# Kernel optimization log

Hardware: AMD Instinct MI355X
Metric: run time of the kernel (lower is better)

## Reference

```python
import jax, jax.numpy as jnp
import numpy as np

B, N = 4, 20                        # batch, qubits
L = int(np.ceil(np.log2(N)))        # 5 layers, one 4x4 generator each


def setup_inputs():
    key = jax.random.key(0)
    k1, k2, k3, k4 = jax.random.split(key, 4)
    psi_re = jax.random.normal(k1, (B, 2 ** N), dtype=jnp.float32)
    psi_im = jax.random.normal(k2, (B, 2 ** N), dtype=jnp.float32)
    nrm = jnp.sqrt(jnp.sum(psi_re ** 2 + psi_im ** 2, axis=1, keepdims=True))
    psi_re, psi_im = psi_re / nrm, psi_im / nrm   # normalized quantum state
    H_re = jax.random.normal(k3, (L, 4, 4), dtype=jnp.float32)
    H_im = jax.random.normal(k4, (L, 4, 4), dtype=jnp.float32)
    return {"psi_re": psi_re, "psi_im": psi_im, "H_re": H_re, "H_im": H_im}


def _make_unitary(A):
    # torch.matrix_exp(A - A^H): expm of an anti-Hermitian generator via eigh
    G = A - A.conj().T
    w, V = jnp.linalg.eigh(-1j * G)            # G = i * Hermitian
    return (V * jnp.exp(1j * w)) @ V.conj().T  # expm(G), unitary


def _apply_gate(T, U4, axes):
    # contract 4x4 gate (reshaped [2,2,2,2]) onto two qubit axes of tensor T
    T = jnp.tensordot(U4, T, axes=((2, 3), axes))
    return jnp.moveaxis(T, (0, 1), axes)


def _gate_pairs(nq):
    pairs = [(2 * i, 2 * i + 1) for i in range(nq // 2)]
    if nq > 2:
        pairs += [(2 * i + 1, (2 * i + 2) % nq) for i in range(nq // 2)]
    return pairs


def _forward(psi_re, psi_im, H_re, H_im):
    psi = (psi_re + 1j * psi_im).astype(jnp.complex64).reshape((B,) + (2,) * N)
    H = (H_re + 1j * H_im).astype(jnp.complex64)
    state, is_dm, nq = psi, False, N
    for layer in range(L):
        U = _make_unitary(H[layer]).reshape(2, 2, 2, 2)
        Uc = U.conj()
        # _2local_conv: brick pattern of the same 2-qubit gate
        for (a, b) in _gate_pairs(nq):
            state = _apply_gate(state, U, (1 + a, 1 + b))
            if is_dm:  # density matrix: also apply U* on bra axes
                state = _apply_gate(state, Uc, (1 + nq + a, 1 + nq + b))
        # _2local_pool: measuring qubits 0..nq//2-1 with index shifting removes
        # the even-indexed qubits -> partial trace over them
        if nq >= 2:
            traced = [2 * i for i in range(nq // 2)]
            kept = [q for q in range(nq) if q not in traced]
            t, k = len(traced), len(kept)
            if is_dm:
                perm = (0,) + tuple(1 + q for q in kept) + tuple(1 + q for q in traced) \
                     + tuple(1 + nq + q for q in kept) + tuple(1 + nq + q for q in traced)
                r = jnp.transpose(state, perm).reshape(B, 2 ** k, 2 ** t, 2 ** k, 2 ** t)
                state = jnp.einsum('bitjt->bij', r).reshape((B,) + (2,) * k + (2,) * k)
            else:
                perm = (0,) + tuple(1 + q for q in traced) + tuple(1 + q for q in kept)
                p = jnp.transpose(state, perm).reshape(B, 2 ** t, 2 ** k)
                state = jnp.einsum('bti,btj->bij', p, p.conj()).reshape((B,) + (2,) * k + (2,) * k)
                is_dm = True
            nq = k
    # final state.measure(0): reduced 1-qubit density matrix, take P(outcome 0)
    r = state.reshape(B, 2, 2 ** (nq - 1), 2, 2 ** (nq - 1))
    rho0 = jnp.einsum('birjr->bij', r)
    return rho0[:, 0, 0].real


def reference(psi_re, psi_im, H_re, H_im):
    return _forward(psi_re, psi_im, H_re, H_im)
```

## Files before the change

### kernel.cpp

```cpp
#include <hip/hip_runtime.h>
#include <math.h>


__device__ __forceinline__ float2 cmul(float2 a, float2 b) {
  return make_float2(a.x * b.x - a.y * b.y, a.x * b.y + a.y * b.x);
}
__device__ __forceinline__ float2 cmadd(float2 acc, float2 a, float2 b) {
  acc.x = fmaf(a.x, b.x, fmaf(-a.y, b.y, acc.x));
  acc.y = fmaf(a.x, b.y, fmaf(a.y, b.x, acc.y));
  return acc;
}
__device__ __forceinline__ float2 cmaddc(float2 acc, float2 a, float2 b) {
  acc.x = fmaf(a.x, b.x, fmaf(a.y, b.y, acc.x));
  acc.y = fmaf(a.y, b.x, fmaf(-a.x, b.y, acc.y));
  return acc;
}
__device__ __forceinline__ int pad(int e) { return e + (e >> 4); }

__device__ __forceinline__ unsigned spread(unsigned v) {
  v = (v | (v << 8)) & 0x00FF00FFu;
  v = (v | (v << 4)) & 0x0F0F0F0Fu;
  v = (v | (v << 2)) & 0x33333333u;
  v = (v | (v << 1)) & 0x55555555u;
  return v;
}
__device__ __forceinline__ unsigned spread2(unsigned v) { return spread(spread(v)); }
__device__ __forceinline__ int ins(int x, int p) {
  return ((x >> p) << (p + 1)) | (x & ((1 << p) - 1));
}

__device__ __forceinline__ void gate4(float2& v0, float2& v1, float2& v2, float2& v3,
                                      const float2 (&U)[16]) {
  float2 n0 = cmul(U[0], v0);  n0 = cmadd(n0, U[1], v1);  n0 = cmadd(n0, U[2], v2);  n0 = cmadd(n0, U[3], v3);
  float2 n1 = cmul(U[4], v0);  n1 = cmadd(n1, U[5], v1);  n1 = cmadd(n1, U[6], v2);  n1 = cmadd(n1, U[7], v3);
  float2 n2 = cmul(U[8], v0);  n2 = cmadd(n2, U[9], v1);  n2 = cmadd(n2, U[10], v2); n2 = cmadd(n2, U[11], v3);
  float2 n3 = cmul(U[12], v0); n3 = cmadd(n3, U[13], v1); n3 = cmadd(n3, U[14], v2); n3 = cmadd(n3, U[15], v3);
  v0 = n0; v1 = n1; v2 = n2; v3 = n3;
}

__device__ __forceinline__ void gate16(float2 (&v)[16], const float2 (&U)[16]) {
#pragma unroll
  for (int g = 0; g < 4; g++)
    gate4(v[g * 4 + 0], v[g * 4 + 1], v[g * 4 + 2], v[g * 4 + 3], U);
#pragma unroll
  for (int lo = 0; lo < 4; lo++)
    gate4(v[lo], v[lo + 4], v[lo + 8], v[lo + 12], U);
}

__device__ __forceinline__ void apply_gate_tile13(float2* t, const float2 (&U)[16],
                                                  int pa, int pb, int tid) {
  int p0 = pa < pb ? pa : pb;
  int p1 = pa < pb ? pb : pa;
  int m0 = (1 << p0) - 1, m1 = (1 << p1) - 1;
  int ia = 1 << pa, ib = 1 << pb;
#pragma unroll
  for (int g = tid; g < 2048; g += 256) {
    int idx = ((g & ~m0) << 1) | (g & m0);
    idx = ((idx & ~m1) << 1) | (idx & m1);
    int e0 = pad(idx), e1 = pad(idx | ib), e2 = pad(idx | ia), e3 = pad(idx | ia | ib);
    float2 v0 = t[e0], v1 = t[e1], v2 = t[e2], v3 = t[e3];
    gate4(v0, v1, v2, v3, U);
    t[e0] = v0; t[e1] = v1; t[e2] = v2; t[e3] = v3;
  }
}

__device__ __forceinline__ void phase4_l0(float2* t, const float2 (&U)[16],
                                          int p0, int p1, int p2, int p3, int tid) {
  int o0 = 1 << p0, o1 = 1 << p1, o2 = 1 << p2, o3 = 1 << p3;
#pragma unroll
  for (int it = 0; it < 2; it++) {
    int h = tid + it * 256;
    int idx = ins(ins(ins(ins(h, p0), p1), p2), p3);
    float2 v[16];
#pragma unroll
    for (int j = 0; j < 16; j++) {
      int off = ((j & 1) ? o0 : 0) + ((j & 2) ? o1 : 0) + ((j & 4) ? o2 : 0) + ((j & 8) ? o3 : 0);
      v[j] = t[pad(idx + off)];
    }
    gate16(v, U);
#pragma unroll
    for (int j = 0; j < 16; j++) {
      int off = ((j & 1) ? o0 : 0) + ((j & 2) ? o1 : 0) + ((j & 4) ? o2 : 0) + ((j & 8) ? o3 : 0);
      t[pad(idx + off)] = v[j];
    }
  }
}

__device__ __forceinline__ void phase4_pool(float2* w, const float2 (&U)[16],
                                            int a_lo, int a_hi, int c_lo, int c_hi,
                                            int o0, int o1, int o2, int o3, int tid) {
#pragma unroll
  for (int it = 0; it < 2; it++) {
    int h = tid + it * 256;
    int uu = h & 7, ss = (h >> 3) & 7, t_lo = h >> 6;
    int u = ins(ins(uu, a_lo), a_hi);
    int s = ins(ins(ss, c_lo), c_hi);
    int base = t_lo * 1056 + s * 33 + u;
    float2 v[16];
#pragma unroll
    for (int j = 0; j < 16; j++) {
      int off = ((j & 1) ? o0 : 0) + ((j & 2) ? o1 : 0) + ((j & 4) ? o2 : 0) + ((j & 8) ? o3 : 0);
      v[j] = w[base + off];
    }
    gate16(v, U);
#pragma unroll
    for (int j = 0; j < 16; j++) {
      int off = ((j & 1) ? o0 : 0) + ((j & 2) ? o1 : 0) + ((j & 4) ? o2 : 0) + ((j & 8) ? o3 : 0);
      w[base + off] = v[j];
    }
  }
}

__device__ __forceinline__ void gate_su(float2* w, const float2 (&U)[16],
                                        int a, int c, int offa, int offb, int tid) {
#pragma unroll
  for (int g = tid; g < 2048; g += 256) {
    int uu = g & 15, ss = (g >> 4) & 15, t_lo = g >> 8;
    int u = ins(uu, a), s = ins(ss, c);
    int base = t_lo * 1056 + s * 33 + u;
    float2 v0 = w[base], v1 = w[base + offb], v2 = w[base + offa], v3 = w[base + offa + offb];
    gate4(v0, v1, v2, v3, U);
    w[base] = v0; w[base + offb] = v1; w[base + offa] = v2; w[base + offa + offb] = v3;
  }
}

__global__ __launch_bounds__(320) void expm_kernel(const float* __restrict__ Hre,
                                                   const float* __restrict__ Him,
                                                   float2* __restrict__ Uout) {
  int wave = threadIdx.x >> 6;
  int lane = threadIdx.x & 63;
  if (wave >= 5 || lane >= 16) return;
  int l = wave;
  int r = lane >> 2, c = lane & 3;
  double tr = (double)Hre[l * 16 + r * 4 + c] - (double)Hre[l * 16 + c * 4 + r];
  double ti = (double)Him[l * 16 + r * 4 + c] + (double)Him[l * 16 + c * 4 + r];
  double a = sqrt(tr * tr + ti * ti);
  a += __shfl_xor(a, 1, 64);
  a += __shfl_xor(a, 2, 64);
  double nrm = fmax(a, __shfl_xor(a, 4, 64));
  nrm = fmax(nrm, __shfl_xor(nrm, 8, 64));
  int s = 0;
  while (nrm > 0.25 && s < 60) { nrm *= 0.5; s++; }
  double sc = ldexp(1.0, -s);
  tr *= sc; ti *= sc;
  double id = (r == c) ? 1.0 : 0.0;
  double er = id, ei = 0.0, pr = id, pi = 0.0;
  for (int k = 1; k <= 16; k++) {
    double qr = 0.0, qi = 0.0;
#pragma unroll
    for (int m = 0; m < 4; m++) {
      double pmr = __shfl(pr, r * 4 + m, 64);
      double pmi = __shfl(pi, r * 4 + m, 64);
      double tmr = __shfl(tr, m * 4 + c, 64);
      double tmi = __shfl(ti, m * 4 + c, 64);
      qr = fma(pmr, tmr, fma(-pmi, tmi, qr));
      qi = fma(pmr, tmi, fma(pmi, tmr, qi));
    }
    double inv = 1.0 / (double)k;
    pr = qr * inv; pi = qi * inv;
    er += pr; ei += pi;
  }
  for (int it = 0; it < s; it++) {
    double qr = 0.0, qi = 0.0;
#pragma unroll
    for (int m = 0; m < 4; m++) {
      double amr = __shfl(er, r * 4 + m, 64);
      double ami = __shfl(ei, r * 4 + m, 64);
      double bmr = __shfl(er, m * 4 + c, 64);
      double bmi = __shfl(ei, m * 4 + c, 64);
      qr = fma(amr, bmr, fma(-ami, bmi, qr));
      qi = fma(amr, bmi, fma(ami, bmr, qi));
    }
    er = qr; ei = qi;
  }
  Uout[l * 16 + lane] = make_float2((float)er, (float)ei);
}

__global__ __launch_bounds__(256) void l0_pass1(const float* __restrict__ pre,
                                                const float* __restrict__ pim,
                                                const float2* __restrict__ Umat,
                                                float2* __restrict__ state) {
  extern __shared__ float2 tile[];
  int tid = threadIdx.x;
  int bid = blockIdx.x;
  int b = bid >> 7, hi = bid & 127;
  size_t base = ((size_t)b << 20) | ((size_t)hi << 13);
  float2 U[16];
#pragma unroll
  for (int k = 0; k < 16; k++) U[k] = Umat[k];
  for (int e = tid; e < 8192; e += 256)
    tile[pad(e)] = make_float2(pre[base + e], pim[base + e]);
  __syncthreads();
  phase4_l0(tile, U, 0, 1, 2, 3, tid);   __syncthreads();
  phase4_l0(tile, U, 4, 5, 6, 7, tid);   __syncthreads();
  phase4_l0(tile, U, 8, 9, 10, 11, tid); __syncthreads();
  phase4_l0(tile, U, 1, 2, 3, 4, tid);   __syncthreads();
  phase4_l0(tile, U, 5, 6, 7, 8, tid);   __syncthreads();
  apply_gate_tile13(tile, U, 10, 9, tid); __syncthreads();
  for (int e = tid; e < 8192; e += 256) state[base + e] = tile[pad(e)];
}

__global__ __launch_bounds__(256) void l0_pass2(const float2* __restrict__ Umat,
                                                float2* __restrict__ state) {
  extern __shared__ float2 tile[];
  int tid = threadIdx.x;
  int bid = blockIdx.x;
  int b = bid >> 7, mid = bid & 127;
  size_t base = ((size_t)b << 20) | ((size_t)mid << 4);
  float2 U[16];
#pragma unroll
  for (int k = 0; k < 16; k++) U[k] = Umat[k];
  for (int e = tid; e < 8192; e += 256) {
    size_t a = base + (((size_t)(e >> 4)) << 11) + (size_t)(e & 15);
    tile[pad(e)] = state[a];
  }
  __syncthreads();
  phase4_l0(tile, U, 5, 6, 7, 8, tid);    __syncthreads();
  phase4_l0(tile, U, 9, 10, 11, 12, tid); __syncthreads();
  phase4_l0(tile, U, 4, 5, 6, 7, tid);    __syncthreads();
  phase4_l0(tile, U, 8, 9, 10, 11, tid);  __syncthreads();
  apply_gate_tile13(tile, U, 0, 12, tid); __syncthreads();
  for (int e = tid; e < 8192; e += 256) {
    size_t a = base + (((size_t)(e >> 4)) << 11) + (size_t)(e & 15);
    state[a] = tile[pad(e)];
  }
}

__global__ __launch_bounds__(256) void pool_l1(const float2* __restrict__ Umat,
                                               const float2* __restrict__ state,
                                               float2* __restrict__ partial) {
  extern __shared__ float2 w[];
  int tid = threadIdx.x;
  int bid = blockIdx.x;
  int b = bid >> 7, thi = bid & 127;
  size_t bbase = (size_t)b << 20;
  float2 U[16];
#pragma unroll
  for (int k = 0; k < 16; k++) U[k] = Umat[16 + k];
  unsigned tbase = spread((unsigned)(thi << 3)) << 1;
  for (int e = tid; e < 8192; e += 256) {
    int u = e & 31, s = (e >> 5) & 31, t_lo = e >> 10;
    unsigned addr = tbase | (spread((unsigned)t_lo) << 1) | spread2((unsigned)u)
                  | (spread2((unsigned)s) << 2);
    w[t_lo * 1056 + s * 33 + u] = state[bbase + (size_t)addr];
  }
  __syncthreads();
  phase4_pool(w, U, 3, 4, 3, 4, 8, 264, 16, 528, tid);  __syncthreads();
  phase4_pool(w, U, 1, 2, 1, 2, 2, 66, 4, 132, tid);    __syncthreads();
  gate_su(w, U, 0, 0, 33, 1, tid);                      __syncthreads();
  phase4_pool(w, U, 3, 4, 2, 3, 132, 8, 264, 16, tid);  __syncthreads();
  phase4_pool(w, U, 1, 2, 0, 1, 33, 2, 66, 4, tid);     __syncthreads();
  gate_su(w, U, 0, 4, 1, 528, tid);                     __syncthreads();
  int wv = tid >> 6, lane = tid & 63;
  int u0 = (lane >> 3) << 2, v0 = (lane & 7) << 2;
  float2 acc[4][4];
#pragma unroll
  for (int i = 0; i < 4; i++)
#pragma unroll
    for (int j = 0; j < 4; j++) acc[i][j] = make_float2(0.f, 0.f);
  for (int tl = 0; tl < 2; tl++) {
    int tb = (wv * 2 + tl) * 1056;
#pragma unroll 4
    for (int s = 0; s < 32; s++) {
      int row = tb + s * 33;
      float2 x[4], y[4];
#pragma unroll
      for (int i = 0; i < 4; i++) { x[i] = w[row + u0 + i]; y[i] = w[row + v0 + i]; }
#pragma unroll
      for (int i = 0; i < 4; i++)
#pragma unroll
        for (int j = 0; j < 4; j++) acc[i][j] = cmaddc(acc[i][j], x[i], y[j]);
    }
  }
  __syncthreads();
  if (wv > 0) {
#pragma unroll
    for (int i = 0; i < 4; i++)
#pragma unroll
      for (int j = 0; j < 4; j++)
        w[(wv - 1) * 1024 + (u0 + i) * 32 + (v0 + j)] = acc[i][j];
  }
  __syncthreads();
  if (wv == 0) {
    float2* outp = partial + ((size_t)bid << 10);
#pragma unroll
    for (int i = 0; i < 4; i++)
#pragma unroll
      for (int j = 0; j < 4; j++) {
        float2 a = acc[i][j];
#pragma unroll
        for (int k = 0; k < 3; k++) {
          float2 o = w[k * 1024 + (u0 + i) * 32 + (v0 + j)];
          a.x += o.x; a.y += o.y;
        }
        outp[(u0 + i) * 32 + (v0 + j)] = a;
      }
  }
}

__global__ __launch_bounds__(256) void reduce_partials(const float* __restrict__ partial,
                                                       float* __restrict__ rho32) {
  int idx = blockIdx.x * 256 + threadIdx.x;
  int b = idx >> 11, p = idx & 2047;
  float acc = 0.f;
#pragma unroll 4
  for (int h = 0; h < 128; h++) acc += partial[(((size_t)(b * 128 + h)) << 11) + (size_t)p];
  rho32[idx] = acc;
}

__global__ __launch_bounds__(256) void finish(const float2* __restrict__ Umat,
                                              const float2* __restrict__ rho32,
                                              float* __restrict__ out) {
  __shared__ float2 rho[1024];
  __shared__ float2 r3[64];
  __shared__ float2 r4[16];
  int tid = threadIdx.x;
  int b = blockIdx.x;
  for (int p = tid; p < 1024; p += 256) rho[p] = rho32[(b << 10) + p];
  __syncthreads();

  float2 U[16], Uc[16];
#pragma unroll
  for (int k = 0; k < 16; k++) { U[k] = Umat[32 + k]; Uc[k] = make_float2(U[k].x, -U[k].y); }
  const int gl2[4][2] = {{4,3},{2,1},{3,2},{1,0}};
#pragma unroll
  for (int gi = 0; gi < 4; gi++) {
    int pa = gl2[gi][0], pb = gl2[gi][1];
    int p0 = pa < pb ? pa : pb, p1 = pa < pb ? pb : pa;
    int m0 = (1 << p0) - 1, m1 = (1 << p1) - 1;
    int ia = 1 << pa, ib = 1 << pb;
    {
      int j = tid >> 3, g = tid & 7;
      int idx = ((g & ~m0) << 1) | (g & m0);
      idx = ((idx & ~m1) << 1) | (idx & m1);
      float2 v0 = rho[idx * 32 + j], v1 = rho[(idx | ib) * 32 + j];
      float2 v2 = rho[(idx | ia) * 32 + j], v3 = rho[(idx | ia | ib) * 32 + j];
      gate4(v0, v1, v2, v3, U);
      rho[idx * 32 + j] = v0; rho[(idx | ib) * 32 + j] = v1;
      rho[(idx | ia) * 32 + j] = v2; rho[(idx | ia | ib) * 32 + j] = v3;
    }
    __syncthreads();
    {
      int i = tid >> 3, g = tid & 7;
      int idx = ((g & ~m0) << 1) | (g & m0);
      idx = ((idx & ~m1) << 1) | (idx & m1);
      float2 v0 = rho[i * 32 + idx], v1 = rho[i * 32 + (idx | ib)];
      float2 v2 = rho[i * 32 + (idx | ia)], v3 = rho[i * 32 + (idx | ia | ib)];
      gate4(v0, v1, v2, v3, Uc);
      rho[i * 32 + idx] = v0; rho[i * 32 + (idx | ib)] = v1;
      rho[i * 32 + (idx | ia)] = v2; rho[i * 32 + (idx | ia | ib)] = v3;
    }
    __syncthreads();
  }
  if (tid < 64) {
    int u = tid >> 3, v = tid & 7;
    float2 acc = {0.f, 0.f};
#pragma unroll
    for (int s = 0; s < 4; s++) {
      int iu = ((s >> 1) << 4) | ((u >> 2) << 3) | ((s & 1) << 2) | (((u >> 1) & 1) << 1) | (u & 1);
      int iv = ((s >> 1) << 4) | ((v >> 2) << 3) | ((s & 1) << 2) | (((v >> 1) & 1) << 1) | (v & 1);
      float2 x = rho[iu * 32 + iv];
      acc.x += x.x; acc.y += x.y;
    }
    r3[u * 8 + v] = acc;
  }
  __syncthreads();

#pragma unroll
  for (int k = 0; k < 16; k++) { U[k] = Umat[48 + k]; Uc[k] = make_float2(U[k].x, -U[k].y); }
  const int gl3[2][2] = {{2,1},{1,0}};
#pragma unroll
  for (int gi = 0; gi < 2; gi++) {
    int pa = gl3[gi][0], pb = gl3[gi][1];
    int p0 = pa < pb ? pa : pb, p1 = pa < pb ? pb : pa;
    int m0 = (1 << p0) - 1, m1 = (1 << p1) - 1;
    int ia = 1 << pa, ib = 1 << pb;
    if (tid < 16) {
      int j = tid >> 1, g = tid & 1;
      int idx = ((g & ~m0) << 1) | (g & m0);
      idx = ((idx & ~m1) << 1) | (idx & m1);
      float2 v0 = r3[idx * 8 + j], v1 = r3[(idx | ib) * 8 + j];
      float2 v2 = r3[(idx | ia) * 8 + j], v3 = r3[(idx | ia | ib) * 8 + j];
      gate4(v0, v1, v2, v3, U);
      r3[idx * 8 + j] = v0; r3[(idx | ib) * 8 + j] = v1;
      r3[(idx | ia) * 8 + j] = v2; r3[(idx | ia | ib) * 8 + j] = v3;
    }
    __syncthreads();
    if (tid < 16) {
      int i = tid >> 1, g = tid & 1;
      int idx = ((g & ~m0) << 1) | (g & m0);
      idx = ((idx & ~m1) << 1) | (idx & m1);
      float2 v0 = r3[i * 8 + idx], v1 = r3[i * 8 + (idx | ib)];
      float2 v2 = r3[i * 8 + (idx | ia)], v3 = r3[i * 8 + (idx | ia | ib)];
      gate4(v0, v1, v2, v3, Uc);
      r3[i * 8 + idx] = v0; r3[i * 8 + (idx | ib)] = v1;
      r3[i * 8 + (idx | ia)] = v2; r3[i * 8 + (idx | ia | ib)] = v3;
    }
    __syncthreads();
  }
  if (tid < 16) {
    int u = tid >> 2, v = tid & 3;
    float2 acc = {0.f, 0.f};
#pragma unroll
    for (int s = 0; s < 2; s++) {
      float2 x = r3[((s << 2) | u) * 8 + ((s << 2) | v)];
      acc.x += x.x; acc.y += x.y;
    }
    r4[u * 4 + v] = acc;
  }
  __syncthreads();

#pragma unroll
  for (int k = 0; k < 16; k++) { U[k] = Umat[64 + k]; Uc[k] = make_float2(U[k].x, -U[k].y); }
  if (tid < 4) {
    int j = tid;
    float2 v0 = r4[0 * 4 + j], v1 = r4[1 * 4 + j], v2 = r4[2 * 4 + j], v3 = r4[3 * 4 + j];
    gate4(v0, v1, v2, v3, U);
    r4[0 * 4 + j] = v0; r4[1 * 4 + j] = v1; r4[2 * 4 + j] = v2; r4[3 * 4 + j] = v3;
  }
  __syncthreads();
  if (tid < 4) {
    int i = tid;
    float2 v0 = r4[i * 4 + 0], v1 = r4[i * 4 + 1], v2 = r4[i * 4 + 2], v3 = r4[i * 4 + 3];
    gate4(v0, v1, v2, v3, Uc);
    r4[i * 4 + 0] = v0; r4[i * 4 + 1] = v1; r4[i * 4 + 2] = v2; r4[i * 4 + 3] = v3;
  }
  __syncthreads();
  if (tid == 0) out[b] = r4[0].x + r4[10].x;
}

extern "C" void kernel_launch(void* const* d_in, const int* in_sizes, int n_in,
                              void* d_out, int out_size, void* d_ws, size_t ws_size,
                              hipStream_t stream) {
  const float* psi_re = (const float*)d_in[0];
  const float* psi_im = (const float*)d_in[1];
  const float* H_re = (const float*)d_in[2];
  const float* H_im = (const float*)d_in[3];
  float* out = (float*)d_out;

  char* ws = (char*)d_ws;
  float2* Umat = (float2*)ws;
  float2* state = (float2*)(ws + 4096);
  float* partial = (float*)(ws + 4096 + ((size_t)1 << 25));
  float* rho32 = (float*)(ws + 4096 + ((size_t)1 << 25) + ((size_t)1 << 22));

  const size_t LDS_L0 = 8704 * sizeof(float2);
  const size_t LDS_POOL = 8448 * sizeof(float2);

  hipLaunchKernelGGL(expm_kernel, dim3(1), dim3(320), 0, stream, H_re, H_im, Umat);
  hipLaunchKernelGGL(l0_pass1, dim3(512), dim3(256), LDS_L0, stream,
                     psi_re, psi_im, Umat, state);
  hipLaunchKernelGGL(l0_pass2, dim3(512), dim3(256), LDS_L0, stream, Umat, state);
  hipLaunchKernelGGL(pool_l1, dim3(512), dim3(256), LDS_POOL, stream,
                     Umat, state, (float2*)partial);
  hipLaunchKernelGGL(reduce_partials, dim3(32), dim3(256), 0, stream, partial, rho32);
  hipLaunchKernelGGL(finish, dim3(4), dim3(256), 0, stream, Umat, (const float2*)rho32, out);
}
```

Before: 205.0 us.

## Apply more gates per register-resident pass and fold partial reduction into finish

Gate application in the layer-0 and pool kernels is regrouped so each LDS round trip applies three gates on a 4-qubit group instead of two. This removes one LDS pass per kernel along with its barrier. The standalone reduce_partials kernel is dropped, and the finish kernel now sums the 128 partials itself, saving a launch and an intermediate buffer. The cost is that finish runs only 4 blocks, each serially reading 128x2048 floats, which may make it slow and latency-bound.

```diff
diff --git a/kernel.cpp b/kernel.cpp
--- a/kernel.cpp
+++ b/kernel.cpp
@@ -38,13 +38,23 @@
   v0 = n0; v1 = n1; v2 = n2; v3 = n3;
 }
 
-__device__ __forceinline__ void gate16(float2 (&v)[16], const float2 (&U)[16]) {
+template <int NG>
+__device__ __forceinline__ void gate16n(float2 (&v)[16], const float2 (&U)[16]) {
 #pragma unroll
   for (int g = 0; g < 4; g++)
     gate4(v[g * 4 + 0], v[g * 4 + 1], v[g * 4 + 2], v[g * 4 + 3], U);
 #pragma unroll
   for (int lo = 0; lo < 4; lo++)
     gate4(v[lo], v[lo + 4], v[lo + 8], v[lo + 12], U);
+  if (NG == 3) {
+#pragma unroll
+    for (int b3 = 0; b3 < 2; b3++)
+#pragma unroll
+      for (int b0 = 0; b0 < 2; b0++) {
+        int j = b3 * 8 + b0;
+        gate4(v[j], v[j + 2], v[j + 4], v[j + 6], U);
+      }
+  }
 }
 
 __device__ __forceinline__ void apply_gate_tile13(float2* t, const float2 (&U)[16],
@@ -64,6 +74,7 @@
   }
 }
 
+template <int NG>
 __device__ __forceinline__ void phase4_l0(float2* t, const float2 (&U)[16],
                                           int p0, int p1, int p2, int p3, int tid) {
   int o0 = 1 << p0, o1 = 1 << p1, o2 = 1 << p2, o3 = 1 << p3;
@@ -77,7 +88,7 @@
       int off = ((j & 1) ? o0 : 0) + ((j & 2) ? o1 : 0) + ((j & 4) ? o2 : 0) + ((j & 8) ? o3 : 0);
       v[j] = t[pad(idx + off)];
     }
-    gate16(v, U);
+    gate16n<NG>(v, U);
 #pragma unroll
     for (int j = 0; j < 16; j++) {
       int off = ((j & 1) ? o0 : 0) + ((j & 2) ? o1 : 0) + ((j & 4) ? o2 : 0) + ((j & 8) ? o3 : 0);
@@ -86,6 +97,7 @@
   }
 }
 
+template <int NG>
 __device__ __forceinline__ void phase4_pool(float2* w, const float2 (&U)[16],
                                             int a_lo, int a_hi, int c_lo, int c_hi,
                                             int o0, int o1, int o2, int o3, int tid) {
@@ -102,7 +114,7 @@
       int off = ((j & 1) ? o0 : 0) + ((j & 2) ? o1 : 0) + ((j & 4) ? o2 : 0) + ((j & 8) ? o3 : 0);
       v[j] = w[base + off];
     }
-    gate16(v, U);
+    gate16n<NG>(v, U);
 #pragma unroll
     for (int j = 0; j < 16; j++) {
       int off = ((j & 1) ? o0 : 0) + ((j & 2) ? o1 : 0) + ((j & 4) ? o2 : 0) + ((j & 8) ? o3 : 0);
@@ -111,16 +123,25 @@
   }
 }
 
-__device__ __forceinline__ void gate_su(float2* w, const float2 (&U)[16],
-                                        int a, int c, int offa, int offb, int tid) {
-#pragma unroll
-  for (int g = tid; g < 2048; g += 256) {
-    int uu = g & 15, ss = (g >> 4) & 15, t_lo = g >> 8;
-    int u = ins(uu, a), s = ins(ss, c);
-    int base = t_lo * 1056 + s * 33 + u;
-    float2 v0 = w[base], v1 = w[base + offb], v2 = w[base + offa], v3 = w[base + offa + offb];
-    gate4(v0, v1, v2, v3, U);
-    w[base] = v0; w[base + offb] = v1; w[base + offa] = v2; w[base + offa + offb] = v3;
+__device__ __forceinline__ void pool_p3(float2* w, const float2 (&U)[16], int tid) {
+#pragma unroll
+  for (int it = 0; it < 4; it++) {
+    int h = tid + it * 256;
+    int uu = h & 7, ss = (h >> 3) & 15, t_lo = h >> 7;
+    int base = t_lo * 1056 + (ss << 1) * 33 + (uu << 2);
+    float2 v[8];
+    v[0] = w[base];      v[1] = w[base + 1];
+    v[4] = w[base + 2];  v[5] = w[base + 3];
+    v[2] = w[base + 33]; v[3] = w[base + 34];
+    v[6] = w[base + 35]; v[7] = w[base + 36];
+    gate4(v[0], v[1], v[2], v[3], U);
+    gate4(v[4], v[5], v[6], v[7], U);
+    gate4(v[0], v[2], v[4], v[6], U);
+    gate4(v[1], v[3], v[5], v[7], U);
+    w[base] = v[0];      w[base + 1] = v[1];
+    w[base + 2] = v[4];  w[base + 3] = v[5];
+    w[base + 33] = v[2]; w[base + 34] = v[3];
+    w[base + 35] = v[6]; w[base + 36] = v[7];
   }
 }
 
@@ -191,12 +212,10 @@
   for (int e = tid; e < 8192; e += 256)
     tile[pad(e)] = make_float2(pre[base + e], pim[base + e]);
   __syncthreads();
-  phase4_l0(tile, U, 0, 1, 2, 3, tid);   __syncthreads();
-  phase4_l0(tile, U, 4, 5, 6, 7, tid);   __syncthreads();
-  phase4_l0(tile, U, 8, 9, 10, 11, tid); __syncthreads();
-  phase4_l0(tile, U, 1, 2, 3, 4, tid);   __syncthreads();
-  phase4_l0(tile, U, 5, 6, 7, 8, tid);   __syncthreads();
-  apply_gate_tile13(tile, U, 10, 9, tid); __syncthreads();
+  phase4_l0<3>(tile, U, 0, 1, 2, 3, tid);   __syncthreads();
+  phase4_l0<3>(tile, U, 4, 5, 6, 7, tid);   __syncthreads();
+  phase4_l0<3>(tile, U, 8, 9, 10, 11, tid); __syncthreads();
+  phase4_l0<2>(tile, U, 3, 4, 7, 8, tid);   __syncthreads();
   for (int e = tid; e < 8192; e += 256) state[base + e] = tile[pad(e)];
 }
 
@@ -215,11 +234,10 @@
     tile[pad(e)] = state[a];
   }
   __syncthreads();
-  phase4_l0(tile, U, 5, 6, 7, 8, tid);    __syncthreads();
-  phase4_l0(tile, U, 9, 10, 11, 12, tid); __syncthreads();
-  phase4_l0(tile, U, 4, 5, 6, 7, tid);    __syncthreads();
-  phase4_l0(tile, U, 8, 9, 10, 11, tid);  __syncthreads();
-  apply_gate_tile13(tile, U, 0, 12, tid); __syncthreads();
+  phase4_l0<3>(tile, U, 5, 6, 7, 8, tid);    __syncthreads();
+  phase4_l0<3>(tile, U, 9, 10, 11, 12, tid); __syncthreads();
+  phase4_l0<2>(tile, U, 4, 5, 8, 9, tid);    __syncthreads();
+  apply_gate_tile13(tile, U, 0, 12, tid);    __syncthreads();
   for (int e = tid; e < 8192; e += 256) {
     size_t a = base + (((size_t)(e >> 4)) << 11) + (size_t)(e & 15);
     state[a] = tile[pad(e)];
@@ -245,12 +263,10 @@
     w[t_lo * 1056 + s * 33 + u] = state[bbase + (size_t)addr];
   }
   __syncthreads();
-  phase4_pool(w, U, 3, 4, 3, 4, 8, 264, 16, 528, tid);  __syncthreads();
-  phase4_pool(w, U, 1, 2, 1, 2, 2, 66, 4, 132, tid);    __syncthreads();
-  gate_su(w, U, 0, 0, 33, 1, tid);                      __syncthreads();
-  phase4_pool(w, U, 3, 4, 2, 3, 132, 8, 264, 16, tid);  __syncthreads();
-  phase4_pool(w, U, 1, 2, 0, 1, 33, 2, 66, 4, tid);     __syncthreads();
-  gate_su(w, U, 0, 4, 1, 528, tid);                     __syncthreads();
+  phase4_pool<3>(w, U, 3, 4, 3, 4, 8, 264, 16, 528, tid); __syncthreads();
+  phase4_pool<3>(w, U, 1, 2, 1, 2, 2, 66, 4, 132, tid);   __syncthreads();
+  pool_p3(w, U, tid);                                     __syncthreads();
+  phase4_pool<2>(w, U, 0, 3, 2, 4, 132, 8, 528, 1, tid);  __syncthreads();
   int wv = tid >> 6, lane = tid & 63;
   int u0 = (lane >> 3) << 2, v0 = (lane & 7) << 2;
   float2 acc[4][4];
@@ -298,25 +314,23 @@
   }
 }
 
-__global__ __launch_bounds__(256) void reduce_partials(const float* __restrict__ partial,
-                                                       float* __restrict__ rho32) {
-  int idx = blockIdx.x * 256 + threadIdx.x;
-  int b = idx >> 11, p = idx & 2047;
-  float acc = 0.f;
-#pragma unroll 4
-  for (int h = 0; h < 128; h++) acc += partial[(((size_t)(b * 128 + h)) << 11) + (size_t)p];
-  rho32[idx] = acc;
-}
-
 __global__ __launch_bounds__(256) void finish(const float2* __restrict__ Umat,
-                                              const float2* __restrict__ rho32,
+                                              const float* __restrict__ partial,
                                               float* __restrict__ out) {
   __shared__ float2 rho[1024];
-  __shared__ float2 r3[64];
-  __shared__ float2 r4[16];
+  __shared__ float2 r3s[64];
+  __shared__ float2 r4s[16];
   int tid = threadIdx.x;
   int b = blockIdx.x;
-  for (int p = tid; p < 1024; p += 256) rho[p] = rho32[(b << 10) + p];
+  float* rt = (float*)rho;
+#pragma unroll
+  for (int k = 0; k < 8; k++) {
+    int p = tid + k * 256;
+    float acc = 0.f;
+    for (int h = 0; h < 128; h++)
+      acc += partial[(((size_t)(b * 128 + h)) << 11) + (size_t)p];
+    rt[p] = acc;
+  }
   __syncthreads();
 
   float2 U[16], Uc[16];
@@ -362,7 +376,7 @@
       float2 x = rho[iu * 32 + iv];
       acc.x += x.x; acc.y += x.y;
     }
-    r3[u * 8 + v] = acc;
+    r3s[u * 8 + v] = acc;
   }
   __syncthreads();
 
@@ -379,22 +393,22 @@
       int j = tid >> 1, g = tid & 1;
       int idx = ((g & ~m0) << 1) | (g & m0);
       idx = ((idx & ~m1) << 1) | (idx & m1);
-      float2 v0 = r3[idx * 8 + j], v1 = r3[(idx | ib) * 8 + j];
-      float2 v2 = r3[(idx | ia) * 8 + j], v3 = r3[(idx | ia | ib) * 8 + j];
+      float2 v0 = r3s[idx * 8 + j], v1 = r3s[(idx | ib) * 8 + j];
+      float2 v2 = r3s[(idx | ia) * 8 + j], v3 = r3s[(idx | ia | ib) * 8 + j];
       gate4(v0, v1, v2, v3, U);
-      r3[idx * 8 + j] = v0; r3[(idx | ib) * 8 + j] = v1;
-      r3[(idx | ia) * 8 + j] = v2; r3[(idx | ia | ib) * 8 + j] = v3;
+      r3s[idx * 8 + j] = v0; r3s[(idx | ib) * 8 + j] = v1;
+      r3s[(idx | ia) * 8 + j] = v2; r3s[(idx | ia | ib) * 8 + j] = v3;
     }
     __syncthreads();
     if (tid < 16) {
       int i = tid >> 1, g = tid & 1;
       int idx = ((g & ~m0) << 1) | (g & m0);
       idx = ((idx & ~m1) << 1) | (idx & m1);
-      float2 v0 = r3[i * 8 + idx], v1 = r3[i * 8 + (idx | ib)];
-      float2 v2 = r3[i * 8 + (idx | ia)], v3 = r3[i * 8 + (idx | ia | ib)];
+      float2 v0 = r3s[i * 8 + idx], v1 = r3s[i * 8 + (idx | ib)];
+      float2 v2 = r3s[i * 8 + (idx | ia)], v3 = r3s[i * 8 + (idx | ia | ib)];
       gate4(v0, v1, v2, v3, Uc);
-      r3[i * 8 + idx] = v0; r3[i * 8 + (idx | ib)] = v1;
-      r3[i * 8 + (idx | ia)] = v2; r3[i * 8 + (idx | ia | ib)] = v3;
+      r3s[i * 8 + idx] = v0; r3s[i * 8 + (idx | ib)] = v1;
+      r3s[i * 8 + (idx | ia)] = v2; r3s[i * 8 + (idx | ia | ib)] = v3;
     }
     __syncthreads();
   }
@@ -403,10 +417,10 @@
     float2 acc = {0.f, 0.f};
 #pragma unroll
     for (int s = 0; s < 2; s++) {
-      float2 x = r3[((s << 2) | u) * 8 + ((s << 2) | v)];
+      float2 x = r3s[((s << 2) | u) * 8 + ((s << 2) | v)];
       acc.x += x.x; acc.y += x.y;
     }
-    r4[u * 4 + v] = acc;
+    r4s[u * 4 + v] = acc;
   }
   __syncthreads();
 
@@ -414,19 +428,19 @@
   for (int k = 0; k < 16; k++) { U[k] = Umat[64 + k]; Uc[k] = make_float2(U[k].x, -U[k].y); }
   if (tid < 4) {
     int j = tid;
-    float2 v0 = r4[0 * 4 + j], v1 = r4[1 * 4 + j], v2 = r4[2 * 4 + j], v3 = r4[3 * 4 + j];
+    float2 v0 = r4s[0 * 4 + j], v1 = r4s[1 * 4 + j], v2 = r4s[2 * 4 + j], v3 = r4s[3 * 4 + j];
     gate4(v0, v1, v2, v3, U);
-    r4[0 * 4 + j] = v0; r4[1 * 4 + j] = v1; r4[2 * 4 + j] = v2; r4[3 * 4 + j] = v3;
+    r4s[0 * 4 + j] = v0; r4s[1 * 4 + j] = v1; r4s[2 * 4 + j] = v2; r4s[3 * 4 + j] = v3;
   }
   __syncthreads();
   if (tid < 4) {
     int i = tid;
-    float2 v0 = r4[i * 4 + 0], v1 = r4[i * 4 + 1], v2 = r4[i * 4 + 2], v3 = r4[i * 4 + 3];
+    float2 v0 = r4s[i * 4 + 0], v1 = r4s[i * 4 + 1], v2 = r4s[i * 4 + 2], v3 = r4s[i * 4 + 3];
     gate4(v0, v1, v2, v3, Uc);
-    r4[i * 4 + 0] = v0; r4[i * 4 + 1] = v1; r4[i * 4 + 2] = v2; r4[i * 4 + 3] = v3;
-  }
-  __syncthreads();
-  if (tid == 0) out[b] = r4[0].x + r4[10].x;
+    r4s[i * 4 + 0] = v0; r4s[i * 4 + 1] = v1; r4s[i * 4 + 2] = v2; r4s[i * 4 + 3] = v3;
+  }
+  __syncthreads();
+  if (tid == 0) out[b] = r4s[0].x + r4s[10].x;
 }
 
 extern "C" void kernel_launch(void* const* d_in, const int* in_sizes, int n_in,
@@ -442,7 +456,6 @@
   float2* Umat = (float2*)ws;
   float2* state = (float2*)(ws + 4096);
   float* partial = (float*)(ws + 4096 + ((size_t)1 << 25));
-  float* rho32 = (float*)(ws + 4096 + ((size_t)1 << 25) + ((size_t)1 << 22));
 
   const size_t LDS_L0 = 8704 * sizeof(float2);
   const size_t LDS_POOL = 8448 * sizeof(float2);
@@ -453,6 +466,5 @@
   hipLaunchKernelGGL(l0_pass2, dim3(512), dim3(256), LDS_L0, stream, Umat, state);
   hipLaunchKernelGGL(pool_l1, dim3(512), dim3(256), LDS_POOL, stream,
                      Umat, state, (float2*)partial);
-  hipLaunchKernelGGL(reduce_partials, dim3(32), dim3(256), 0, stream, partial, rho32);
-  hipLaunchKernelGGL(finish, dim3(4), dim3(256), 0, stream, Umat, (const float2*)rho32, out);
-}
+  hipLaunchKernelGGL(finish, dim3(4), dim3(256), 0, stream, Umat, partial, out);
+}
```

Result: slower. 236.4 us (+15.4%).
